# Optimization experiments

Hardware: AMD Instinct MI355X
Metric: run time of the kernel (lower is better)

## Reference

```python
import jax, jax.numpy as jnp
import numpy as np


def setup_inputs() -> dict:
    B, I, H = 4096, 512, 1024
    key = jax.random.key(0)
    ks = jax.random.split(key, 10)
    return {
        "input": jax.random.normal(ks[0], (B, I), dtype=jnp.float32),
        "t": jax.random.uniform(ks[1], (B, 1), dtype=jnp.float32),
        "hx": jax.random.normal(ks[2], (B, H), dtype=jnp.float32),
        "cx": jax.random.normal(ks[3], (B, H), dtype=jnp.float32),
        "weight_ih": jax.random.normal(ks[4], (4 * H, I), dtype=jnp.float32),
        "weight_hh": jax.random.normal(ks[5], (4 * H, H), dtype=jnp.float32),
        "bias_ih": jax.random.normal(ks[6], (4 * H,), dtype=jnp.float32),
        "bias_hh": jax.random.normal(ks[7], (4 * H,), dtype=jnp.float32),
        "W_decomp": jax.random.normal(ks[8], (H, H), dtype=jnp.float32),
        "b_decomp": jax.random.normal(ks[9], (H,), dtype=jnp.float32),
    }


def reference(input, t, hx, cx, weight_ih, weight_hh, bias_ih, bias_hh, W_decomp, b_decomp):
    H = W_decomp.shape[0]
    # gates: [B, 4H]
    gates = input @ weight_ih.T + bias_ih + hx @ weight_hh.T + bias_hh
    ingate, forgetgate, cellgate, outgate = jnp.split(gates, 4, axis=1)
    # time-decay factor g(t): elementwise 1/t where t != 0, broadcast [B,1] -> [B,H]
    T = jnp.where(t != 0, 1.0 / jnp.where(t != 0, t, 1.0), 0.0)  # [B, 1]
    T = jnp.broadcast_to(T, (t.shape[0], H))
    # T-LSTM cell-state decomposition
    C_ST = jnp.tanh(cx @ W_decomp + b_decomp)
    cx_adj = cx - C_ST + T * C_ST
    ingate = jax.nn.sigmoid(ingate)
    forgetgate = jax.nn.sigmoid(forgetgate)
    cellgate = jnp.tanh(cellgate)
    outgate = jax.nn.sigmoid(outgate)
    cy = forgetgate * cx_adj + ingate * cellgate
    hy = outgate * jnp.tanh(cy)
    return (hy, cy)
```

## Files before the change

### kernel.cpp

```cpp
#include <hip/hip_runtime.h>
#include <cstdint>


typedef __attribute__((ext_vector_type(8))) __bf16 bf16x8;
typedef __attribute__((ext_vector_type(4))) float f32x4;

__device__ __forceinline__ unsigned short f2bf_rn(float f) {
  unsigned int u = __float_as_uint(f);
  unsigned int r = u + 0x7fffu + ((u >> 16) & 1u);
  return (unsigned short)(r >> 16);
}
__device__ __forceinline__ float bf2f(unsigned short h) {
  return __uint_as_float(((unsigned int)h) << 16);
}
__device__ __forceinline__ float sigm_f(float x) {
  return 1.0f / (1.0f + __expf(-x));
}
__device__ __forceinline__ float tanh_f(float x) {
  return 1.0f - 2.0f / (__expf(2.0f * x) + 1.0f);
}
__device__ __forceinline__ void gl_lds16(const void* g, void* l) {
  __builtin_amdgcn_global_load_lds(
      (const __attribute__((address_space(1))) void*)g,
      (__attribute__((address_space(3))) void*)l, 16, 0, 0);
}

__global__ __launch_bounds__(384) void prep_k(
    const float* __restrict__ input, const float* __restrict__ hx,
    const float* __restrict__ w_ih, const float* __restrict__ w_hh,
    const float* __restrict__ cx, const float* __restrict__ Wd,
    unsigned short* __restrict__ Xhi, unsigned short* __restrict__ Xlo,
    unsigned short* __restrict__ Whi, unsigned short* __restrict__ Wlo,
    unsigned short* __restrict__ Chi, unsigned short* __restrict__ Clo,
    unsigned short* __restrict__ Dhi, unsigned short* __restrict__ Dlo) {
  const int bid = blockIdx.x;
  if (bid >= 12288) {
    __shared__ float tile[64][65];
    const int tb = bid - 12288;
    const int bx = (tb & 15) * 64;
    const int by = (tb >> 4) * 64;
    const int tx = threadIdx.x & 63;
    const int ty = threadIdx.x >> 6;
    for (int r = ty; r < 64; r += 6)
      tile[r][tx] = Wd[(long)(by + r) * 1024 + bx + tx];
    __syncthreads();
    for (int r = ty; r < 64; r += 6) {
      float v = tile[tx][r];
      unsigned short h = f2bf_rn(v);
      long o = (long)(bx + r) * 1024 + by + tx;
      Dhi[o] = h;
      Dlo[o] = f2bf_rn(v - bf2f(h));
    }
    return;
  }
  const int k = threadIdx.x << 2;
  const float* src;
  unsigned short *hi, *lo;
  if (bid < 4096) {
    const long m = bid;
    src = (k < 512) ? (input + m * 512 + k) : (hx + m * 1024 + (k - 512));
    hi = Xhi + m * 1536 + k;
    lo = Xlo + m * 1536 + k;
  } else if (bid < 8192) {
    const int n = bid - 4096;
    const int g = n >> 10;
    const int h = n & 1023;
    const long nd = ((long)(h >> 4) << 6) | (g << 4) | (h & 15);
    src = (k < 512) ? (w_ih + (long)n * 512 + k) : (w_hh + (long)n * 1024 + (k - 512));
    hi = Whi + nd * 1536 + k;
    lo = Wlo + nd * 1536 + k;
  } else {
    if (k >= 1024) return;
    const long m = bid - 8192;
    src = cx + m * 1024 + k;
    hi = Chi + m * 1024 + k;
    lo = Clo + m * 1024 + k;
  }
  float4 v = *(const float4*)src;
  ushort4 hv, lv;
  hv.x = f2bf_rn(v.x); lv.x = f2bf_rn(v.x - bf2f(hv.x));
  hv.y = f2bf_rn(v.y); lv.y = f2bf_rn(v.y - bf2f(hv.y));
  hv.z = f2bf_rn(v.z); lv.z = f2bf_rn(v.z - bf2f(hv.z));
  hv.w = f2bf_rn(v.w); lv.w = f2bf_rn(v.w - bf2f(hv.w));
  *(ushort4*)hi = hv;
  *(ushort4*)lo = lv;
}

__global__ __launch_bounds__(256) void gemm_mega(
    const unsigned short* __restrict__ Xh, const unsigned short* __restrict__ Xl,
    const unsigned short* __restrict__ Wh, const unsigned short* __restrict__ Wl,
    const unsigned short* __restrict__ Ch, const unsigned short* __restrict__ Cl,
    const unsigned short* __restrict__ Dh, const unsigned short* __restrict__ Dl,
    const float* __restrict__ b_ih, const float* __restrict__ b_hh,
    const float* __restrict__ b_d, const float* __restrict__ cx,
    const float* __restrict__ t, float* __restrict__ out) {
  __shared__ __align__(16) unsigned short sAh[128 * 32];
  __shared__ __align__(16) unsigned short sAl[128 * 32];
  __shared__ __align__(16) unsigned short sBh[128 * 32];
  __shared__ __align__(16) unsigned short sBl[128 * 32];

  const int n_blk = blockIdx.x & 31;
  const int m_blk = blockIdx.x >> 5;
  const int m0 = m_blk * 128;
  const int n0 = n_blk * 128;
  const int h0 = n_blk * 32;

  const int tid = threadIdx.x;
  const int wave = tid >> 6;
  const int lane = tid & 63;
  const int wr = wave >> 1;
  const int wc = wave & 1;
  const int srow = lane >> 2;
  const int ssw = (((lane & 3) ^ ((lane >> 3) & 3)) << 3);
  const int fm = lane & 15;
  const int fq = lane >> 4;
  const int psw = (fq ^ ((fm >> 1) & 3)) << 3;

  unsigned short* const dA0h = sAh + (wave * 16) * 32;
  unsigned short* const dA0l = sAl + (wave * 16) * 32;
  unsigned short* const dA1h = sAh + (64 + wave * 16) * 32;
  unsigned short* const dA1l = sAl + (64 + wave * 16) * 32;
  unsigned short* const dB0h = sBh + (wave * 16) * 32;
  unsigned short* const dB0l = sBl + (wave * 16) * 32;
  unsigned short* const dB1h = sBh + (64 + wave * 16) * 32;
  unsigned short* const dB1l = sBl + (64 + wave * 16) * 32;

  f32x4 dacc[4];
#pragma unroll
  for (int i = 0; i < 4; ++i) dacc[i] = {0.f, 0.f, 0.f, 0.f};

  {
    const long aoff = (long)(m0 + wave * 16 + srow) * 1024 + ssw;
    const unsigned short* pAh0 = Ch + aoff;
    const unsigned short* pAl0 = Cl + aoff;
    const unsigned short* pAh1 = pAh0 + 64 * 1024;
    const unsigned short* pAl1 = pAl0 + 64 * 1024;
    const unsigned short* pD =
        ((wave & 2) ? Dl : Dh) + (long)(h0 + (wave & 1) * 16 + srow) * 1024 + ssw;
    unsigned short* const dD = ((wave & 2) ? sBl : sBh) + ((wave & 1) * 16) * 32;

    for (int kt = 0; kt < 1024; kt += 128) {
#pragma unroll
      for (int kk = 0; kk < 4; ++kk) {
        gl_lds16(pAh0 + kk * 32, dA0h);
        gl_lds16(pAl0 + kk * 32, dA0l);
        gl_lds16(pAh1 + kk * 32, dA1h);
        gl_lds16(pAl1 + kk * 32, dA1l);
        gl_lds16(pD + kk * 32, dD);
        __syncthreads();
        bf16x8 ah[4], al[4];
#pragma unroll
        for (int mf = 0; mf < 4; ++mf) {
          const int ao = (wr * 64 + mf * 16 + fm) * 32 + psw;
          ah[mf] = *(const bf16x8*)(sAh + ao);
          al[mf] = *(const bf16x8*)(sAl + ao);
        }
        const int bo = (wc * 16 + fm) * 32 + psw;
        const bf16x8 bh = *(const bf16x8*)(sBh + bo);
        const bf16x8 bl = *(const bf16x8*)(sBl + bo);
#pragma unroll
        for (int mf = 0; mf < 4; ++mf) {
          dacc[mf] = __builtin_amdgcn_mfma_f32_16x16x32_bf16(ah[mf], bh, dacc[mf], 0, 0, 0);
          dacc[mf] = __builtin_amdgcn_mfma_f32_16x16x32_bf16(ah[mf], bl, dacc[mf], 0, 0, 0);
          dacc[mf] = __builtin_amdgcn_mfma_f32_16x16x32_bf16(al[mf], bh, dacc[mf], 0, 0, 0);
        }
        __syncthreads();
      }
      pAh0 += 128; pAl0 += 128; pAh1 += 128; pAl1 += 128; pD += 128;
    }
  }

  f32x4 acc[4][4];
#pragma unroll
  for (int i = 0; i < 4; ++i)
#pragma unroll
    for (int j = 0; j < 4; ++j) acc[i][j] = {0.f, 0.f, 0.f, 0.f};

  {
    const long aoff = (long)(m0 + wave * 16 + srow) * 1536 + ssw;
    const long boff = (long)(n0 + wave * 16 + srow) * 1536 + ssw;
    const unsigned short* pXh0 = Xh + aoff;
    const unsigned short* pXl0 = Xl + aoff;
    const unsigned short* pXh1 = pXh0 + 64 * 1536;
    const unsigned short* pXl1 = pXl0 + 64 * 1536;
    const unsigned short* pWh0 = Wh + boff;
    const unsigned short* pWl0 = Wl + boff;
    const unsigned short* pWh1 = pWh0 + 64 * 1536;
    const unsigned short* pWl1 = pWl0 + 64 * 1536;

    for (int kt = 0; kt < 1536; kt += 128) {
#pragma unroll
      for (int kk = 0; kk < 4; ++kk) {
        gl_lds16(pXh0 + kk * 32, dA0h);
        gl_lds16(pXl0 + kk * 32, dA0l);
        gl_lds16(pXh1 + kk * 32, dA1h);
        gl_lds16(pXl1 + kk * 32, dA1l);
        gl_lds16(pWh0 + kk * 32, dB0h);
        gl_lds16(pWl0 + kk * 32, dB0l);
        gl_lds16(pWh1 + kk * 32, dB1h);
        gl_lds16(pWl1 + kk * 32, dB1l);
        __syncthreads();
        bf16x8 ah[4], al[4], bh[4], bl[4];
#pragma unroll
        for (int mf = 0; mf < 4; ++mf) {
          const int ao = (wr * 64 + mf * 16 + fm) * 32 + psw;
          ah[mf] = *(const bf16x8*)(sAh + ao);
          al[mf] = *(const bf16x8*)(sAl + ao);
        }
#pragma unroll
        for (int nf = 0; nf < 4; ++nf) {
          const int bo = (wc * 64 + nf * 16 + fm) * 32 + psw;
          bh[nf] = *(const bf16x8*)(sBh + bo);
          bl[nf] = *(const bf16x8*)(sBl + bo);
        }
#pragma unroll
        for (int nf = 0; nf < 4; ++nf)
#pragma unroll
          for (int mf = 0; mf < 4; ++mf) {
            acc[mf][nf] = __builtin_amdgcn_mfma_f32_16x16x32_bf16(ah[mf], bh[nf], acc[mf][nf], 0, 0, 0);
            acc[mf][nf] = __builtin_amdgcn_mfma_f32_16x16x32_bf16(ah[mf], bl[nf], acc[mf][nf], 0, 0, 0);
            acc[mf][nf] = __builtin_amdgcn_mfma_f32_16x16x32_bf16(al[mf], bh[nf], acc[mf][nf], 0, 0, 0);
          }
        __syncthreads();
      }
      pXh0 += 128; pXl0 += 128; pXh1 += 128; pXl1 += 128;
      pWh0 += 128; pWl0 += 128; pWh1 += 128; pWl1 += 128;
    }
  }

  const int h = h0 + wc * 16 + fm;
  const float bi  = b_ih[h]        + b_hh[h];
  const float bff = b_ih[1024 + h] + b_hh[1024 + h];
  const float bg  = b_ih[2048 + h] + b_hh[2048 + h];
  const float bo2 = b_ih[3072 + h] + b_hh[3072 + h];
  const float bd  = b_d[h];
#pragma unroll
  for (int mf = 0; mf < 4; ++mf) {
#pragma unroll
    for (int r = 0; r < 4; ++r) {
      const int m = m0 + wr * 64 + mf * 16 + fq * 4 + r;
      const float tv = t[m];
      const float T = (tv != 0.0f) ? (1.0f / tv) : 0.0f;
      const float cst = tanh_f(dacc[mf][r] + bd);
      const float cadj = cx[(long)m * 1024 + h] + (T - 1.0f) * cst;
      const float ig = sigm_f(acc[mf][0][r] + bi);
      const float fg = sigm_f(acc[mf][1][r] + bff);
      const float cg = tanh_f(acc[mf][2][r] + bg);
      const float og = sigm_f(acc[mf][3][r] + bo2);
      const float cyv = fg * cadj + ig * cg;
      const float hyv = og * tanh_f(cyv);
      out[(long)m * 1024 + h] = hyv;
      out[4096L * 1024 + (long)m * 1024 + h] = cyv;
    }
  }
}

extern "C" void kernel_launch(void* const* d_in, const int* in_sizes, int n_in,
                              void* d_out, int out_size, void* d_ws, size_t ws_size,
                              hipStream_t stream) {
  const float* input = (const float*)d_in[0];
  const float* t     = (const float*)d_in[1];
  const float* hx    = (const float*)d_in[2];
  const float* cx    = (const float*)d_in[3];
  const float* w_ih  = (const float*)d_in[4];
  const float* w_hh  = (const float*)d_in[5];
  const float* b_ih  = (const float*)d_in[6];
  const float* b_hh  = (const float*)d_in[7];
  const float* Wd    = (const float*)d_in[8];
  const float* b_d   = (const float*)d_in[9];

  const long B = 4096, H = 1024, KX = 1536, NG = 4096;

  char* ws = (char*)d_ws;
  unsigned short* Xhi = (unsigned short*)ws; ws += B * KX * 2;
  unsigned short* Xlo = (unsigned short*)ws; ws += B * KX * 2;
  unsigned short* Whi = (unsigned short*)ws; ws += NG * KX * 2;
  unsigned short* Wlo = (unsigned short*)ws; ws += NG * KX * 2;
  unsigned short* Chi = (unsigned short*)ws; ws += B * H * 2;
  unsigned short* Clo = (unsigned short*)ws; ws += B * H * 2;
  unsigned short* Dhi = (unsigned short*)ws; ws += H * H * 2;
  unsigned short* Dlo = (unsigned short*)ws; ws += H * H * 2;

  prep_k<<<12544, 384, 0, stream>>>(input, hx, w_ih, w_hh, cx, Wd,
                                    Xhi, Xlo, Whi, Wlo, Chi, Clo, Dhi, Dlo);
  gemm_mega<<<1024, 256, 0, stream>>>(Xhi, Xlo, Whi, Wlo, Chi, Clo, Dhi, Dlo,
                                      b_ih, b_hh, b_d, cx, t, (float*)d_out);
}
```

Baseline: 327.8 us.

## Switch gate GEMM to 32x32x16 MFMA tiles with shuffle-based epilogue remap

Replaces the 4x4 grid of 16x16x32 bf16 MFMAs in the main gate GEMM with a 2x2 grid of 32x32x16 MFMAs per wave. This halves the LDS fragment reads per k-step and uses the larger instruction, which has higher operand reuse. The accumulator layout no longer matches the gate/column mapping or the decomposition accumulator layout, so the epilogue uses cross-lane shuffles to regroup the four gates and the C_ST values per lane. That adds shuffle work and precomputed swizzled offsets, and raises the register footprint.

```diff
diff --git a/kernel.cpp b/kernel.cpp
--- a/kernel.cpp
+++ b/kernel.cpp
@@ -4,6 +4,7 @@
 
 typedef __attribute__((ext_vector_type(8))) __bf16 bf16x8;
 typedef __attribute__((ext_vector_type(4))) float f32x4;
+typedef __attribute__((ext_vector_type(16))) float f32x16;
 
 __device__ __forceinline__ unsigned short f2bf_rn(float f) {
   unsigned int u = __float_as_uint(f);
@@ -115,6 +116,8 @@
   const int fm = lane & 15;
   const int fq = lane >> 4;
   const int psw = (fq ^ ((fm >> 1) & 3)) << 3;
+  const int col = lane & 31;
+  const int hi5 = lane >> 5;
 
   unsigned short* const dA0h = sAh + (wave * 16) * 32;
   unsigned short* const dA0l = sAl + (wave * 16) * 32;
@@ -170,11 +173,31 @@
     }
   }
 
-  f32x4 acc[4][4];
-#pragma unroll
-  for (int i = 0; i < 4; ++i)
-#pragma unroll
-    for (int j = 0; j < 4; ++j) acc[i][j] = {0.f, 0.f, 0.f, 0.f};
+  f32x16 acc[2][2];
+#pragma unroll
+  for (int i = 0; i < 2; ++i)
+#pragma unroll
+    for (int j = 0; j < 2; ++j)
+#pragma unroll
+      for (int e = 0; e < 16; ++e) acc[i][j][e] = 0.f;
+
+  int offA[2][2], offB[2][2];
+#pragma unroll
+  for (int mf = 0; mf < 2; ++mf) {
+    const int arow = wr * 64 + mf * 32 + col;
+    const int s = (arow >> 1) & 3;
+#pragma unroll
+    for (int ks = 0; ks < 2; ++ks)
+      offA[mf][ks] = arow * 32 + (((hi5 + 2 * ks) ^ s) << 3);
+  }
+#pragma unroll
+  for (int nf = 0; nf < 2; ++nf) {
+    const int brow = wc * 64 + nf * 32 + col;
+    const int s = (brow >> 1) & 3;
+#pragma unroll
+    for (int ks = 0; ks < 2; ++ks)
+      offB[nf][ks] = brow * 32 + (((hi5 + 2 * ks) ^ s) << 3);
+  }
 
   {
     const long aoff = (long)(m0 + wave * 16 + srow) * 1536 + ssw;
@@ -200,27 +223,34 @@
         gl_lds16(pWh1 + kk * 32, dB1h);
         gl_lds16(pWl1 + kk * 32, dB1l);
         __syncthreads();
-        bf16x8 ah[4], al[4], bh[4], bl[4];
-#pragma unroll
-        for (int mf = 0; mf < 4; ++mf) {
-          const int ao = (wr * 64 + mf * 16 + fm) * 32 + psw;
-          ah[mf] = *(const bf16x8*)(sAh + ao);
-          al[mf] = *(const bf16x8*)(sAl + ao);
-        }
-#pragma unroll
-        for (int nf = 0; nf < 4; ++nf) {
-          const int bo = (wc * 64 + nf * 16 + fm) * 32 + psw;
-          bh[nf] = *(const bf16x8*)(sBh + bo);
-          bl[nf] = *(const bf16x8*)(sBl + bo);
-        }
-#pragma unroll
-        for (int nf = 0; nf < 4; ++nf)
-#pragma unroll
-          for (int mf = 0; mf < 4; ++mf) {
-            acc[mf][nf] = __builtin_amdgcn_mfma_f32_16x16x32_bf16(ah[mf], bh[nf], acc[mf][nf], 0, 0, 0);
-            acc[mf][nf] = __builtin_amdgcn_mfma_f32_16x16x32_bf16(ah[mf], bl[nf], acc[mf][nf], 0, 0, 0);
-            acc[mf][nf] = __builtin_amdgcn_mfma_f32_16x16x32_bf16(al[mf], bh[nf], acc[mf][nf], 0, 0, 0);
+        bf16x8 ah[2][2], al[2][2], bh[2][2], bl[2][2];
+#pragma unroll
+        for (int mf = 0; mf < 2; ++mf)
+#pragma unroll
+          for (int ks = 0; ks < 2; ++ks) {
+            ah[mf][ks] = *(const bf16x8*)(sAh + offA[mf][ks]);
+            al[mf][ks] = *(const bf16x8*)(sAl + offA[mf][ks]);
           }
+#pragma unroll
+        for (int nf = 0; nf < 2; ++nf)
+#pragma unroll
+          for (int ks = 0; ks < 2; ++ks) {
+            bh[nf][ks] = *(const bf16x8*)(sBh + offB[nf][ks]);
+            bl[nf][ks] = *(const bf16x8*)(sBl + offB[nf][ks]);
+          }
+#pragma unroll
+        for (int ks = 0; ks < 2; ++ks)
+#pragma unroll
+          for (int nf = 0; nf < 2; ++nf)
+#pragma unroll
+            for (int mf = 0; mf < 2; ++mf) {
+              acc[mf][nf] = __builtin_amdgcn_mfma_f32_32x32x16_bf16(
+                  ah[mf][ks], bh[nf][ks], acc[mf][nf], 0, 0, 0);
+              acc[mf][nf] = __builtin_amdgcn_mfma_f32_32x32x16_bf16(
+                  ah[mf][ks], bl[nf][ks], acc[mf][nf], 0, 0, 0);
+              acc[mf][nf] = __builtin_amdgcn_mfma_f32_32x32x16_bf16(
+                  al[mf][ks], bh[nf][ks], acc[mf][nf], 0, 0, 0);
+            }
         __syncthreads();
       }
       pXh0 += 128; pXl0 += 128; pXh1 += 128; pXl1 += 128;
@@ -228,30 +258,44 @@
     }
   }
 
-  const int h = h0 + wc * 16 + fm;
+  const int b4 = (lane >> 4) & 1;
+  const int hlow = lane & 15;
+  const int h = h0 + wc * 16 + hlow;
   const float bi  = b_ih[h]        + b_hh[h];
   const float bff = b_ih[1024 + h] + b_hh[1024 + h];
   const float bg  = b_ih[2048 + h] + b_hh[2048 + h];
   const float bo2 = b_ih[3072 + h] + b_hh[3072 + h];
   const float bd  = b_d[h];
 #pragma unroll
-  for (int mf = 0; mf < 4; ++mf) {
-#pragma unroll
-    for (int r = 0; r < 4; ++r) {
-      const int m = m0 + wr * 64 + mf * 16 + fq * 4 + r;
-      const float tv = t[m];
-      const float T = (tv != 0.0f) ? (1.0f / tv) : 0.0f;
-      const float cst = tanh_f(dacc[mf][r] + bd);
-      const float cadj = cx[(long)m * 1024 + h] + (T - 1.0f) * cst;
-      const float ig = sigm_f(acc[mf][0][r] + bi);
-      const float fg = sigm_f(acc[mf][1][r] + bff);
-      const float cg = tanh_f(acc[mf][2][r] + bg);
-      const float og = sigm_f(acc[mf][3][r] + bo2);
-      const float cyv = fg * cadj + ig * cg;
-      const float hyv = og * tanh_f(cyv);
-      out[(long)m * 1024 + h] = hyv;
-      out[4096L * 1024 + (long)m * 1024 + h] = cyv;
-    }
+  for (int reg = 0; reg < 16; ++reg) {
+    const float s0 = b4 ? acc[0][0][reg] : acc[1][0][reg];
+    const float s1 = b4 ? acc[0][1][reg] : acc[1][1][reg];
+    const float r0 = __shfl_xor(s0, 16, 64);
+    const float r1 = __shfl_xor(s1, 16, 64);
+    const float a0 = b4 ? acc[1][0][reg] : acc[0][0][reg];
+    const float a1 = b4 ? acc[1][1][reg] : acc[0][1][reg];
+    const float gi = b4 ? r0 : a0;
+    const float gf = b4 ? a0 : r0;
+    const float gg = b4 ? r1 : a1;
+    const float go = b4 ? a1 : r1;
+    const int lsrc = (((((reg >> 2) & 1) << 1) + hi5) << 4) | hlow;
+    const float d0 = __shfl(dacc[(reg >> 3)][reg & 3], lsrc, 64);
+    const float d1 = __shfl(dacc[2 + (reg >> 3)][reg & 3], lsrc, 64);
+    const float dv = b4 ? d1 : d0;
+
+    const int m = m0 + wr * 64 + b4 * 32 + (reg & 3) + 8 * (reg >> 2) + 4 * hi5;
+    const float tv = t[m];
+    const float T = (tv != 0.0f) ? (1.0f / tv) : 0.0f;
+    const float cst = tanh_f(dv + bd);
+    const float cadj = cx[(long)m * 1024 + h] + (T - 1.0f) * cst;
+    const float ig = sigm_f(gi + bi);
+    const float fg = sigm_f(gf + bff);
+    const float cg = tanh_f(gg + bg);
+    const float og = sigm_f(go + bo2);
+    const float cyv = fg * cadj + ig * cg;
+    const float hyv = og * tanh_f(cyv);
+    out[(long)m * 1024 + h] = hyv;
+    out[4096L * 1024 + (long)m * 1024 + h] = cyv;
   }
 }
 
```

After: 334.6 us. 1.02x slower.

## Drop split-bf16 correction MFMAs except forget/cell gates; coarsen prep blocks

Applied to the files above, without the earlier changes.

The gate GEMM now applies the low-part correction MFMAs selectively. Only the forget-gate fragments keep both cross terms, the cell-gate fragments keep one, and the input and output gates use a single hi×hi product. Only waves 1 and 2 stage the W low parts into LDS, since only those rows are still read. This cuts MFMA work and global-to-LDS traffic, at the cost of reduced precision on the input and output gates. The prep kernel also handles four rows or tiles per block and fuses the cx split into the X rows, reducing the block count.

```diff
diff --git a/kernel.cpp b/kernel.cpp
--- a/kernel.cpp
+++ b/kernel.cpp
@@ -23,6 +23,17 @@
   __builtin_amdgcn_global_load_lds(
       (const __attribute__((address_space(1))) void*)g,
       (__attribute__((address_space(3))) void*)l, 16, 0, 0);
+}
+__device__ __forceinline__ void split4(const float* src,
+                                       unsigned short* hi, unsigned short* lo) {
+  float4 v = *(const float4*)src;
+  ushort4 hv, lv;
+  hv.x = f2bf_rn(v.x); lv.x = f2bf_rn(v.x - bf2f(hv.x));
+  hv.y = f2bf_rn(v.y); lv.y = f2bf_rn(v.y - bf2f(hv.y));
+  hv.z = f2bf_rn(v.z); lv.z = f2bf_rn(v.z - bf2f(hv.z));
+  hv.w = f2bf_rn(v.w); lv.w = f2bf_rn(v.w - bf2f(hv.w));
+  *(ushort4*)hi = hv;
+  *(ushort4*)lo = lv;
 }
 
 __global__ __launch_bounds__(384) void prep_k(
@@ -34,56 +45,52 @@
     unsigned short* __restrict__ Chi, unsigned short* __restrict__ Clo,
     unsigned short* __restrict__ Dhi, unsigned short* __restrict__ Dlo) {
   const int bid = blockIdx.x;
-  if (bid >= 12288) {
+  const int k = threadIdx.x << 2;
+  if (bid >= 2048) {
     __shared__ float tile[64][65];
-    const int tb = bid - 12288;
-    const int bx = (tb & 15) * 64;
-    const int by = (tb >> 4) * 64;
     const int tx = threadIdx.x & 63;
     const int ty = threadIdx.x >> 6;
-    for (int r = ty; r < 64; r += 6)
-      tile[r][tx] = Wd[(long)(by + r) * 1024 + bx + tx];
-    __syncthreads();
-    for (int r = ty; r < 64; r += 6) {
-      float v = tile[tx][r];
-      unsigned short h = f2bf_rn(v);
-      long o = (long)(bx + r) * 1024 + by + tx;
-      Dhi[o] = h;
-      Dlo[o] = f2bf_rn(v - bf2f(h));
+#pragma unroll 1
+    for (int i = 0; i < 4; ++i) {
+      const int tb = (bid - 2048) * 4 + i;
+      const int bx = (tb & 15) * 64;
+      const int by = (tb >> 4) * 64;
+      for (int r = ty; r < 64; r += 6)
+        tile[r][tx] = Wd[(long)(by + r) * 1024 + bx + tx];
+      __syncthreads();
+      for (int r = ty; r < 64; r += 6) {
+        float v = tile[tx][r];
+        unsigned short h = f2bf_rn(v);
+        long o = (long)(bx + r) * 1024 + by + tx;
+        Dhi[o] = h;
+        Dlo[o] = f2bf_rn(v - bf2f(h));
+      }
+      __syncthreads();
     }
     return;
   }
-  const int k = threadIdx.x << 2;
-  const float* src;
-  unsigned short *hi, *lo;
-  if (bid < 4096) {
-    const long m = bid;
-    src = (k < 512) ? (input + m * 512 + k) : (hx + m * 1024 + (k - 512));
-    hi = Xhi + m * 1536 + k;
-    lo = Xlo + m * 1536 + k;
-  } else if (bid < 8192) {
-    const int n = bid - 4096;
-    const int g = n >> 10;
-    const int h = n & 1023;
-    const long nd = ((long)(h >> 4) << 6) | (g << 4) | (h & 15);
-    src = (k < 512) ? (w_ih + (long)n * 512 + k) : (w_hh + (long)n * 1024 + (k - 512));
-    hi = Whi + nd * 1536 + k;
-    lo = Wlo + nd * 1536 + k;
+  if (bid < 1024) {
+#pragma unroll 1
+    for (int i = 0; i < 4; ++i) {
+      const long m = (long)bid * 4 + i;
+      const float* src =
+          (k < 512) ? (input + m * 512 + k) : (hx + m * 1024 + (k - 512));
+      split4(src, Xhi + m * 1536 + k, Xlo + m * 1536 + k);
+      if (k < 1024)
+        split4(cx + m * 1024 + k, Chi + m * 1024 + k, Clo + m * 1024 + k);
+    }
   } else {
-    if (k >= 1024) return;
-    const long m = bid - 8192;
-    src = cx + m * 1024 + k;
-    hi = Chi + m * 1024 + k;
-    lo = Clo + m * 1024 + k;
-  }
-  float4 v = *(const float4*)src;
-  ushort4 hv, lv;
-  hv.x = f2bf_rn(v.x); lv.x = f2bf_rn(v.x - bf2f(hv.x));
-  hv.y = f2bf_rn(v.y); lv.y = f2bf_rn(v.y - bf2f(hv.y));
-  hv.z = f2bf_rn(v.z); lv.z = f2bf_rn(v.z - bf2f(hv.z));
-  hv.w = f2bf_rn(v.w); lv.w = f2bf_rn(v.w - bf2f(hv.w));
-  *(ushort4*)hi = hv;
-  *(ushort4*)lo = lv;
+#pragma unroll 1
+    for (int i = 0; i < 4; ++i) {
+      const int n = (bid - 1024) * 4 + i;
+      const int g = n >> 10;
+      const int h = n & 1023;
+      const long nd = ((long)(h >> 4) << 6) | (g << 4) | (h & 15);
+      const float* src =
+          (k < 512) ? (w_ih + (long)n * 512 + k) : (w_hh + (long)n * 1024 + (k - 512));
+      split4(src, Whi + nd * 1536 + k, Wlo + nd * 1536 + k);
+    }
+  }
 }
 
 __global__ __launch_bounds__(256) void gemm_mega(
@@ -187,6 +194,7 @@
     const unsigned short* pWl0 = Wl + boff;
     const unsigned short* pWh1 = pWh0 + 64 * 1536;
     const unsigned short* pWl1 = pWl0 + 64 * 1536;
+    const bool stage_wl = (wave == 1) | (wave == 2);
 
     for (int kt = 0; kt < 1536; kt += 128) {
 #pragma unroll
@@ -196,11 +204,13 @@
         gl_lds16(pXh1 + kk * 32, dA1h);
         gl_lds16(pXl1 + kk * 32, dA1l);
         gl_lds16(pWh0 + kk * 32, dB0h);
-        gl_lds16(pWl0 + kk * 32, dB0l);
         gl_lds16(pWh1 + kk * 32, dB1h);
-        gl_lds16(pWl1 + kk * 32, dB1l);
+        if (stage_wl) {
+          gl_lds16(pWl0 + kk * 32, dB0l);
+          gl_lds16(pWl1 + kk * 32, dB1l);
+        }
         __syncthreads();
-        bf16x8 ah[4], al[4], bh[4], bl[4];
+        bf16x8 ah[4], al[4], bh[4];
 #pragma unroll
         for (int mf = 0; mf < 4; ++mf) {
           const int ao = (wr * 64 + mf * 16 + fm) * 32 + psw;
@@ -211,15 +221,20 @@
         for (int nf = 0; nf < 4; ++nf) {
           const int bo = (wc * 64 + nf * 16 + fm) * 32 + psw;
           bh[nf] = *(const bf16x8*)(sBh + bo);
-          bl[nf] = *(const bf16x8*)(sBl + bo);
-        }
+        }
+        const bf16x8 bl1 = *(const bf16x8*)(sBl + (wc * 64 + 16 + fm) * 32 + psw);
+        const bf16x8 bl2 = *(const bf16x8*)(sBl + (wc * 64 + 32 + fm) * 32 + psw);
 #pragma unroll
         for (int nf = 0; nf < 4; ++nf)
 #pragma unroll
           for (int mf = 0; mf < 4; ++mf) {
             acc[mf][nf] = __builtin_amdgcn_mfma_f32_16x16x32_bf16(ah[mf], bh[nf], acc[mf][nf], 0, 0, 0);
-            acc[mf][nf] = __builtin_amdgcn_mfma_f32_16x16x32_bf16(ah[mf], bl[nf], acc[mf][nf], 0, 0, 0);
-            acc[mf][nf] = __builtin_amdgcn_mfma_f32_16x16x32_bf16(al[mf], bh[nf], acc[mf][nf], 0, 0, 0);
+            if (nf == 1) {
+              acc[mf][nf] = __builtin_amdgcn_mfma_f32_16x16x32_bf16(ah[mf], bl1, acc[mf][nf], 0, 0, 0);
+              acc[mf][nf] = __builtin_amdgcn_mfma_f32_16x16x32_bf16(al[mf], bh[nf], acc[mf][nf], 0, 0, 0);
+            }
+            if (nf == 2)
+              acc[mf][nf] = __builtin_amdgcn_mfma_f32_16x16x32_bf16(ah[mf], bl2, acc[mf][nf], 0, 0, 0);
           }
         __syncthreads();
       }
@@ -281,8 +296,8 @@
   unsigned short* Dhi = (unsigned short*)ws; ws += H * H * 2;
   unsigned short* Dlo = (unsigned short*)ws; ws += H * H * 2;
 
-  prep_k<<<12544, 384, 0, stream>>>(input, hx, w_ih, w_hh, cx, Wd,
-                                    Xhi, Xlo, Whi, Wlo, Chi, Clo, Dhi, Dlo);
+  prep_k<<<2112, 384, 0, stream>>>(input, hx, w_ih, w_hh, cx, Wd,
+                                   Xhi, Xlo, Whi, Wlo, Chi, Clo, Dhi, Dlo);
   gemm_mega<<<1024, 256, 0, stream>>>(Xhi, Xlo, Whi, Wlo, Chi, Clo, Dhi, Dlo,
                                       b_ih, b_hh, b_d, cx, t, (float*)d_out);
 }
```

New measurement: 316.4 us. 1.04x faster.
